# Performance work log

Measured on AMD Instinct MI355X. Metric: run time of the kernel, lower is better.

Reference implementation:

```python
import jax, jax.numpy as jnp
import numpy as np

B, H, S, D = 4, 16, 2048, 64

def setup_inputs() -> dict:
    key = jax.random.key(0)
    kq, kk, kv = jax.random.split(key, 3)
    query = jax.random.normal(kq, (B, H, S, D), dtype=jnp.float32)
    key_t = jax.random.normal(kk, (B, H, S, D), dtype=jnp.float32)
    value = jax.random.normal(kv, (B, H, S, D), dtype=jnp.float32)
    return {"query": query, "key": key_t, "value": value}

def reference(query, key, value):
    d = query.shape[-1]
    scale = 1.0 / jnp.sqrt(jnp.asarray(d, dtype=query.dtype))
    # scores: [B, H, S_q, S_k]
    scores = jnp.einsum('bhqd,bhkd->bhqk', query, key) * scale
    p_attn = jax.nn.softmax(scores, axis=-1)
    # out: [B, H, S_q, D]
    return jnp.einsum('bhqk,bhkd->bhqd', p_attn, value)
```

## Files before the change

### kernel.cpp

```cpp
#include <hip/hip_runtime.h>
#include <hip/hip_bf16.h>


constexpr int Sdim = 2048;
constexpr int Ddim = 64;
constexpr int QBLK = 64;
constexpr int KVBLK = 64;
constexpr int NW = 4;
constexpr int NBH = 64;
constexpr int NT = Sdim / KVBLK;
constexpr float QSCALE = 0.125f * 1.44269504f;
constexpr float DEFER_THR = 11.0f;

typedef __attribute__((ext_vector_type(8))) short short8;
typedef __attribute__((ext_vector_type(4))) float f32x4;
typedef __attribute__((ext_vector_type(4))) unsigned short ushort4v;
typedef __attribute__((ext_vector_type(2))) unsigned int uint2v;

typedef __attribute__((address_space(1))) const unsigned int GU32;
typedef __attribute__((address_space(3))) unsigned int LU32;

__device__ __forceinline__ unsigned short f2bf(float f) {
    union { float f; unsigned int u; } v; v.f = f;
    unsigned int r = v.u + 0x7FFFu + ((v.u >> 16) & 1u);
    return (unsigned short)(r >> 16);
}

__device__ __forceinline__ unsigned int cvt_pk_bf16(float lo, float hi) {
    unsigned int r;
    asm("v_cvt_pk_bf16_f32 %0, %1, %2" : "=v"(r) : "v"(lo), "v"(hi));
    return r;
}

__device__ __forceinline__ void gload_lds16(const unsigned short* g, unsigned short* l) {
    __builtin_amdgcn_global_load_lds((GU32*)g, (LU32*)l, 16, 0, 0);
}

__global__ __launch_bounds__(256)
void prep_k(const float* __restrict__ Kg, unsigned short* __restrict__ Kbf) {
    size_t idx = ((size_t)blockIdx.x * 256 + threadIdx.x) * 4;
    int c0 = (int)(idx & 63);
    size_t row = idx >> 6;
    int swz = ((int)row & 7) << 3;
    float4 f = *(const float4*)(Kg + idx);
    ushort4v h;
    h.x = f2bf(f.x); h.y = f2bf(f.y); h.z = f2bf(f.z); h.w = f2bf(f.w);
    *(ushort4v*)(Kbf + (row << 6) + (c0 ^ swz)) = h;
}

__global__ __launch_bounds__(256)
void prep_v(const float* __restrict__ Vg, unsigned short* __restrict__ Vtb) {
    int bh = blockIdx.x >> 5, t = blockIdx.x & 31;
    const float* src = Vg + ((size_t)bh * Sdim + t * KVBLK) * Ddim;
    unsigned short* dst = Vtb + ((size_t)bh * NT + t) * (Ddim * KVBLK);
    int kv0 = (threadIdx.x & 15) * 4;
    int d0  = (threadIdx.x >> 4) * 4;
    float v[4][4];
#pragma unroll
    for (int j = 0; j < 4; ++j)
        *(float4*)v[j] = *(const float4*)(src + (size_t)(kv0 + j) * Ddim + d0);
#pragma unroll
    for (int i = 0; i < 4; ++i) {
        int d = d0 + i;
        ushort4v h;
        h.x = f2bf(v[0][i]); h.y = f2bf(v[1][i]);
        h.z = f2bf(v[2][i]); h.w = f2bf(v[3][i]);
        *(ushort4v*)(dst + d * KVBLK + (kv0 ^ ((d & 7) << 3))) = h;
    }
}

__global__ __launch_bounds__(256, 4)
void attn_fwd_fast(const float* __restrict__ Qg, const unsigned short* __restrict__ Kbf,
                   const unsigned short* __restrict__ Vtb, float* __restrict__ Og)
{
    __shared__ unsigned short Kt[KVBLK][Ddim];
    __shared__ unsigned short Vt[Ddim][KVBLK];
    __shared__ unsigned short Pt[NW][16][KVBLK];

    const int tid = threadIdx.x;
    const int w   = tid >> 6;
    const int l   = tid & 63;
    const int g   = l >> 4;
    const int q   = l & 15;
    const int swz = (q & 7) << 3;

    const int bh = blockIdx.y;
    const size_t base = (size_t)bh * Sdim * Ddim;
    const int q0 = blockIdx.x * QBLK;

    short8 qf[2];
    {
        const float* qrow = Qg + base + (size_t)(q0 + w * 16 + q) * Ddim;
#pragma unroll
        for (int kc = 0; kc < 2; ++kc) {
            float fv[8];
            *(float4*)(fv)     = *(const float4*)(qrow + kc * 32 + g * 8);
            *(float4*)(fv + 4) = *(const float4*)(qrow + kc * 32 + g * 8 + 4);
            short8 r;
#pragma unroll
            for (int j = 0; j < 8; ++j) r[j] = (short)f2bf(fv[j] * QSCALE);
            qf[kc] = r;
        }
    }

    f32x4 o[4];
#pragma unroll
    for (int dt = 0; dt < 4; ++dt)
#pragma unroll
        for (int r = 0; r < 4; ++r) o[dt][r] = 0.0f;
    float m_run = -INFINITY, l_run = 0.0f;

    for (int t = 0; t < NT; ++t) {
        __syncthreads();
        {
            const unsigned short* ksrc = Kbf + base + (size_t)t * (KVBLK * Ddim);
            const unsigned short* vsrc = Vtb + base + (size_t)t * (KVBLK * Ddim);
            const int eo = w * 512 + l * 8;
            gload_lds16(ksrc + eo,        &Kt[0][0] + w * 512);
            gload_lds16(ksrc + eo + 2048, &Kt[0][0] + w * 512 + 2048);
            gload_lds16(vsrc + eo,        &Vt[0][0] + w * 512);
            gload_lds16(vsrc + eo + 2048, &Vt[0][0] + w * 512 + 2048);
        }
        __syncthreads();

        f32x4 sa[4];
#pragma unroll
        for (int nt = 0; nt < 4; ++nt)
#pragma unroll
            for (int r = 0; r < 4; ++r) sa[nt][r] = 0.0f;
        __builtin_amdgcn_s_setprio(1);
#pragma unroll
        for (int kc = 0; kc < 2; ++kc)
#pragma unroll
            for (int nt = 0; nt < 4; ++nt) {
                const short8 kf = *(const short8*)&Kt[nt * 16 + q][(kc * 32 + g * 8) ^ swz];
                sa[nt] = __builtin_amdgcn_mfma_f32_16x16x32_bf16(kf, qf[kc], sa[nt], 0, 0, 0);
            }
        __builtin_amdgcn_s_setprio(0);

        float mx = sa[0][0];
#pragma unroll
        for (int nt = 0; nt < 4; ++nt)
#pragma unroll
            for (int r = 0; r < 4; ++r) mx = fmaxf(mx, sa[nt][r]);
        mx = fmaxf(mx, __shfl_xor(mx, 16));
        mx = fmaxf(mx, __shfl_xor(mx, 32));

        float p[4][4];
        float s = 0.0f;
        if (__all(mx - m_run <= DEFER_THR)) {
#pragma unroll
            for (int nt = 0; nt < 4; ++nt)
#pragma unroll
                for (int r = 0; r < 4; ++r) {
                    float e = exp2f(sa[nt][r] - m_run);
                    p[nt][r] = e; s += e;
                }
            s += __shfl_xor(s, 16);
            s += __shfl_xor(s, 32);
            l_run += s;
        } else {
            float mnew = fmaxf(m_run, mx);
            float fr = exp2f(m_run - mnew);
            m_run = mnew;
#pragma unroll
            for (int nt = 0; nt < 4; ++nt)
#pragma unroll
                for (int r = 0; r < 4; ++r) {
                    float e = exp2f(sa[nt][r] - mnew);
                    p[nt][r] = e; s += e;
                }
            s += __shfl_xor(s, 16);
            s += __shfl_xor(s, 32);
            l_run = l_run * fr + s;
            float frb[4];
#pragma unroll
            for (int r = 0; r < 4; ++r) frb[r] = __shfl(fr, 4 * g + r);
#pragma unroll
            for (int dt = 0; dt < 4; ++dt)
#pragma unroll
                for (int r = 0; r < 4; ++r) o[dt][r] *= frb[r];
        }

#pragma unroll
        for (int nt = 0; nt < 4; ++nt) {
            uint2v pp;
            pp.x = cvt_pk_bf16(p[nt][0], p[nt][1]);
            pp.y = cvt_pk_bf16(p[nt][2], p[nt][3]);
            *(uint2v*)&Pt[w][q][(nt * 16 + 4 * g) ^ swz] = pp;
        }

        __builtin_amdgcn_s_setprio(1);
#pragma unroll
        for (int kc = 0; kc < 2; ++kc) {
            const short8 pa = *(const short8*)&Pt[w][q][(kc * 32 + g * 8) ^ swz];
#pragma unroll
            for (int dt = 0; dt < 4; ++dt) {
                const short8 vf = *(const short8*)&Vt[dt * 16 + q][(kc * 32 + g * 8) ^ swz];
                o[dt] = __builtin_amdgcn_mfma_f32_16x16x32_bf16(pa, vf, o[dt], 0, 0, 0);
            }
        }
        __builtin_amdgcn_s_setprio(0);
    }

    float inv = 1.0f / l_run;
    float invb[4];
#pragma unroll
    for (int r = 0; r < 4; ++r) invb[r] = __shfl(inv, 4 * g + r);
#pragma unroll
    for (int r = 0; r < 4; ++r) {
        float* orow = Og + base + (size_t)(q0 + w * 16 + 4 * g + r) * Ddim;
#pragma unroll
        for (int dt = 0; dt < 4; ++dt) orow[dt * 16 + q] = o[dt][r] * invb[r];
    }
}

__global__ __launch_bounds__(256, 4)
void attn_fwd_slow(const float* __restrict__ Qg, const float* __restrict__ Kg,
                   const float* __restrict__ Vg, float* __restrict__ Og)
{
    __shared__ unsigned short Kt[KVBLK][Ddim];
    __shared__ unsigned short Vt[Ddim][KVBLK];
    __shared__ unsigned short Pt[NW][16][KVBLK];

    const int tid = threadIdx.x;
    const int w   = tid >> 6;
    const int l   = tid & 63;
    const int g   = l >> 4;
    const int q   = l & 15;
    const int swz = (q & 7) << 3;

    const size_t base = (size_t)blockIdx.y * Sdim * Ddim;
    const int q0 = blockIdx.x * QBLK;

    short8 qf[2];
    {
        const float* qrow = Qg + base + (size_t)(q0 + w * 16 + q) * Ddim;
#pragma unroll
        for (int kc = 0; kc < 2; ++kc) {
            float fv[8];
            *(float4*)(fv)     = *(const float4*)(qrow + kc * 32 + g * 8);
            *(float4*)(fv + 4) = *(const float4*)(qrow + kc * 32 + g * 8 + 4);
            short8 r;
#pragma unroll
            for (int j = 0; j < 8; ++j) r[j] = (short)f2bf(fv[j] * QSCALE);
            qf[kc] = r;
        }
    }

    f32x4 o[4];
#pragma unroll
    for (int dt = 0; dt < 4; ++dt)
#pragma unroll
        for (int r = 0; r < 4; ++r) o[dt][r] = 0.0f;
    float m_run = -INFINITY, l_run = 0.0f;

    for (int t = 0; t < NT; ++t) {
        __syncthreads();
        {
            const float* Ksrc = Kg + base + (size_t)t * KVBLK * Ddim;
            const float* Vsrc = Vg + base + (size_t)t * KVBLK * Ddim;
#pragma unroll
            for (int it = 0; it < 4; ++it) {
                int idx = it * 1024 + tid * 4;
                int r = idx >> 6, c = idx & 63;
                float4 kf4 = *(const float4*)(Ksrc + idx);
                ushort4v hk;
                hk.x = f2bf(kf4.x); hk.y = f2bf(kf4.y);
                hk.z = f2bf(kf4.z); hk.w = f2bf(kf4.w);
                *(ushort4v*)&Kt[r][c ^ ((r & 7) << 3)] = hk;
            }
            {
                const int d = l;
                const int vswz = (d & 7) << 3;
#pragma unroll
                for (int i = 0; i < 4; ++i) {
                    int kv0 = w * 16 + i * 4;
                    float a0 = Vsrc[(size_t)(kv0 + 0) * Ddim + d];
                    float a1 = Vsrc[(size_t)(kv0 + 1) * Ddim + d];
                    float a2 = Vsrc[(size_t)(kv0 + 2) * Ddim + d];
                    float a3 = Vsrc[(size_t)(kv0 + 3) * Ddim + d];
                    ushort4v hv;
                    hv.x = f2bf(a0); hv.y = f2bf(a1);
                    hv.z = f2bf(a2); hv.w = f2bf(a3);
                    *(ushort4v*)&Vt[d][kv0 ^ vswz] = hv;
                }
            }
        }
        __syncthreads();

        f32x4 sa[4];
#pragma unroll
        for (int nt = 0; nt < 4; ++nt)
#pragma unroll
            for (int r = 0; r < 4; ++r) sa[nt][r] = 0.0f;
#pragma unroll
        for (int kc = 0; kc < 2; ++kc)
#pragma unroll
            for (int nt = 0; nt < 4; ++nt) {
                const short8 kf = *(const short8*)&Kt[nt * 16 + q][(kc * 32 + g * 8) ^ swz];
                sa[nt] = __builtin_amdgcn_mfma_f32_16x16x32_bf16(kf, qf[kc], sa[nt], 0, 0, 0);
            }

        float mx = sa[0][0];
#pragma unroll
        for (int nt = 0; nt < 4; ++nt)
#pragma unroll
            for (int r = 0; r < 4; ++r) mx = fmaxf(mx, sa[nt][r]);
        mx = fmaxf(mx, __shfl_xor(mx, 16));
        mx = fmaxf(mx, __shfl_xor(mx, 32));
        float mnew = fmaxf(m_run, mx);
        float fr = exp2f(m_run - mnew);
        m_run = mnew;

        float p[4][4];
        float s = 0.0f;
#pragma unroll
        for (int nt = 0; nt < 4; ++nt)
#pragma unroll
            for (int r = 0; r < 4; ++r) {
                float e = exp2f(sa[nt][r] - mnew);
                p[nt][r] = e; s += e;
            }
        s += __shfl_xor(s, 16);
        s += __shfl_xor(s, 32);
        l_run = l_run * fr + s;

#pragma unroll
        for (int nt = 0; nt < 4; ++nt) {
            uint2v pp;
            pp.x = cvt_pk_bf16(p[nt][0], p[nt][1]);
            pp.y = cvt_pk_bf16(p[nt][2], p[nt][3]);
            *(uint2v*)&Pt[w][q][(nt * 16 + 4 * g) ^ swz] = pp;
        }

        float frb[4];
#pragma unroll
        for (int r = 0; r < 4; ++r) frb[r] = __shfl(fr, 4 * g + r);
#pragma unroll
        for (int dt = 0; dt < 4; ++dt)
#pragma unroll
            for (int r = 0; r < 4; ++r) o[dt][r] *= frb[r];

#pragma unroll
        for (int kc = 0; kc < 2; ++kc) {
            const short8 pa = *(const short8*)&Pt[w][q][(kc * 32 + g * 8) ^ swz];
#pragma unroll
            for (int dt = 0; dt < 4; ++dt) {
                const short8 vf = *(const short8*)&Vt[dt * 16 + q][(kc * 32 + g * 8) ^ swz];
                o[dt] = __builtin_amdgcn_mfma_f32_16x16x32_bf16(pa, vf, o[dt], 0, 0, 0);
            }
        }
    }

    float inv = 1.0f / l_run;
    float invb[4];
#pragma unroll
    for (int r = 0; r < 4; ++r) invb[r] = __shfl(inv, 4 * g + r);
#pragma unroll
    for (int r = 0; r < 4; ++r) {
        float* orow = Og + base + (size_t)(q0 + w * 16 + 4 * g + r) * Ddim;
#pragma unroll
        for (int dt = 0; dt < 4; ++dt) orow[dt * 16 + q] = o[dt][r] * invb[r];
    }
}

extern "C" void kernel_launch(void* const* d_in, const int* in_sizes, int n_in,
                              void* d_out, int out_size, void* d_ws, size_t ws_size,
                              hipStream_t stream) {
    const float* Q = (const float*)d_in[0];
    const float* K = (const float*)d_in[1];
    const float* V = (const float*)d_in[2];
    float* O = (float*)d_out;
    const size_t elems = (size_t)NBH * Sdim * Ddim;
    const size_t need  = elems * 2 * 2;
    dim3 grid(Sdim / QBLK, NBH);
    if (ws_size >= need) {
        unsigned short* Kbf = (unsigned short*)d_ws;
        unsigned short* Vtb = Kbf + elems;
        prep_k<<<dim3((unsigned)(elems / 4 / 256)), dim3(256), 0, stream>>>(K, Kbf);
        prep_v<<<dim3(NBH * NT), dim3(256), 0, stream>>>(V, Vtb);
        attn_fwd_fast<<<grid, dim3(256), 0, stream>>>(Q, Kbf, Vtb, O);
    } else {
        attn_fwd_slow<<<grid, dim3(256), 0, stream>>>(Q, K, V, O);
    }
}
```

Before: 257.3 us.

## Keep P in registers by permuting V layout, fold max into MFMA init

Re-lays out the transposed V in prep_v, now staged through LDS, so that the S-tile accumulator fragment can be packed directly as the A operand of the PV MFMA. This removes the per-tile P round trip through shared memory and its LDS buffer. The running max is subtracted by seeding the QK accumulator with -m_run, and the row-sum reduction is deferred to the end. Occupancy hint is raised to 8 blocks per CU, which risks register pressure.

```diff
diff --git a/kernel.cpp b/kernel.cpp
--- a/kernel.cpp
+++ b/kernel.cpp
@@ -15,7 +15,6 @@
 typedef __attribute__((ext_vector_type(8))) short short8;
 typedef __attribute__((ext_vector_type(4))) float f32x4;
 typedef __attribute__((ext_vector_type(4))) unsigned short ushort4v;
-typedef __attribute__((ext_vector_type(2))) unsigned int uint2v;
 
 typedef __attribute__((address_space(1))) const unsigned int GU32;
 typedef __attribute__((address_space(3))) unsigned int LU32;
@@ -50,32 +49,46 @@
 
 __global__ __launch_bounds__(256)
 void prep_v(const float* __restrict__ Vg, unsigned short* __restrict__ Vtb) {
+    __shared__ unsigned short Vl[KVBLK][Ddim + 4];
     int bh = blockIdx.x >> 5, t = blockIdx.x & 31;
     const float* src = Vg + ((size_t)bh * Sdim + t * KVBLK) * Ddim;
     unsigned short* dst = Vtb + ((size_t)bh * NT + t) * (Ddim * KVBLK);
-    int kv0 = (threadIdx.x & 15) * 4;
-    int d0  = (threadIdx.x >> 4) * 4;
-    float v[4][4];
-#pragma unroll
-    for (int j = 0; j < 4; ++j)
-        *(float4*)v[j] = *(const float4*)(src + (size_t)(kv0 + j) * Ddim + d0);
-#pragma unroll
-    for (int i = 0; i < 4; ++i) {
-        int d = d0 + i;
-        ushort4v h;
-        h.x = f2bf(v[0][i]); h.y = f2bf(v[1][i]);
-        h.z = f2bf(v[2][i]); h.w = f2bf(v[3][i]);
-        *(ushort4v*)(dst + d * KVBLK + (kv0 ^ ((d & 7) << 3))) = h;
-    }
-}
-
-__global__ __launch_bounds__(256, 4)
+
+    {
+        int kv = threadIdx.x >> 2;
+        int dq = (threadIdx.x & 3) * 16;
+#pragma unroll
+        for (int i = 0; i < 4; ++i) {
+            float4 f = *(const float4*)(src + (size_t)kv * Ddim + dq + 4 * i);
+            ushort4v h;
+            h.x = f2bf(f.x); h.y = f2bf(f.y); h.z = f2bf(f.z); h.w = f2bf(f.w);
+            *(ushort4v*)&Vl[kv][dq + 4 * i] = h;
+        }
+    }
+    __syncthreads();
+    {
+        int d  = threadIdx.x >> 2;
+        int sc = (threadIdx.x & 3) * 16;
+        int swzd = (d & 7) << 3;
+#pragma unroll
+        for (int u = 0; u < 4; ++u) {
+            int s0 = sc + 4 * u;
+            int kc = s0 >> 5, g = (s0 >> 3) & 3, h = (s0 >> 2) & 1;
+            int kvb = 32 * kc + 16 * h + 4 * g;
+            ushort4v o;
+            o.x = Vl[kvb + 0][d]; o.y = Vl[kvb + 1][d];
+            o.z = Vl[kvb + 2][d]; o.w = Vl[kvb + 3][d];
+            *(ushort4v*)(dst + (size_t)d * KVBLK + (s0 ^ swzd)) = o;
+        }
+    }
+}
+
+__global__ __launch_bounds__(256, 8)
 void attn_fwd_fast(const float* __restrict__ Qg, const unsigned short* __restrict__ Kbf,
                    const unsigned short* __restrict__ Vtb, float* __restrict__ Og)
 {
     __shared__ unsigned short Kt[KVBLK][Ddim];
     __shared__ unsigned short Vt[Ddim][KVBLK];
-    __shared__ unsigned short Pt[NW][16][KVBLK];
 
     const int tid = threadIdx.x;
     const int w   = tid >> 6;
@@ -108,7 +121,10 @@
     for (int dt = 0; dt < 4; ++dt)
 #pragma unroll
         for (int r = 0; r < 4; ++r) o[dt][r] = 0.0f;
-    float m_run = -INFINITY, l_run = 0.0f;
+    float m_run = 0.0f;
+    float l_part = 0.0f;
+
+    union PU { unsigned int u[4]; short8 s8; };
 
     for (int t = 0; t < NT; ++t) {
         __syncthreads();
@@ -127,7 +143,7 @@
 #pragma unroll
         for (int nt = 0; nt < 4; ++nt)
 #pragma unroll
-            for (int r = 0; r < 4; ++r) sa[nt][r] = 0.0f;
+            for (int r = 0; r < 4; ++r) sa[nt][r] = -m_run;
         __builtin_amdgcn_s_setprio(1);
 #pragma unroll
         for (int kc = 0; kc < 2; ++kc)
@@ -138,41 +154,39 @@
             }
         __builtin_amdgcn_s_setprio(0);
 
-        float mx = sa[0][0];
-#pragma unroll
-        for (int nt = 0; nt < 4; ++nt)
-#pragma unroll
-            for (int r = 0; r < 4; ++r) mx = fmaxf(mx, sa[nt][r]);
+        f32x4 m4 = sa[0];
+#pragma unroll
+        for (int nt = 1; nt < 4; ++nt)
+#pragma unroll
+            for (int r = 0; r < 4; ++r) m4[r] = fmaxf(m4[r], sa[nt][r]);
+        float mx = fmaxf(fmaxf(m4[0], m4[1]), fmaxf(m4[2], m4[3]));
         mx = fmaxf(mx, __shfl_xor(mx, 16));
         mx = fmaxf(mx, __shfl_xor(mx, 32));
 
-        float p[4][4];
-        float s = 0.0f;
-        if (__all(mx - m_run <= DEFER_THR)) {
-#pragma unroll
-            for (int nt = 0; nt < 4; ++nt)
-#pragma unroll
-                for (int r = 0; r < 4; ++r) {
-                    float e = exp2f(sa[nt][r] - m_run);
-                    p[nt][r] = e; s += e;
-                }
-            s += __shfl_xor(s, 16);
-            s += __shfl_xor(s, 32);
-            l_run += s;
+        PU pa[2];
+        float ts = 0.0f;
+        if (__all(mx <= DEFER_THR)) {
+#pragma unroll
+            for (int nt = 0; nt < 4; ++nt) {
+                float e0 = exp2f(sa[nt][0]), e1 = exp2f(sa[nt][1]);
+                float e2 = exp2f(sa[nt][2]), e3 = exp2f(sa[nt][3]);
+                ts += (e0 + e1) + (e2 + e3);
+                pa[nt >> 1].u[(nt & 1) * 2 + 0] = cvt_pk_bf16(e0, e1);
+                pa[nt >> 1].u[(nt & 1) * 2 + 1] = cvt_pk_bf16(e2, e3);
+            }
+            l_part += ts;
         } else {
-            float mnew = fmaxf(m_run, mx);
-            float fr = exp2f(m_run - mnew);
-            m_run = mnew;
-#pragma unroll
-            for (int nt = 0; nt < 4; ++nt)
-#pragma unroll
-                for (int r = 0; r < 4; ++r) {
-                    float e = exp2f(sa[nt][r] - mnew);
-                    p[nt][r] = e; s += e;
-                }
-            s += __shfl_xor(s, 16);
-            s += __shfl_xor(s, 32);
-            l_run = l_run * fr + s;
+            float fr = exp2f(-mx);
+            m_run += mx;
+#pragma unroll
+            for (int nt = 0; nt < 4; ++nt) {
+                float e0 = exp2f(sa[nt][0] - mx), e1 = exp2f(sa[nt][1] - mx);
+                float e2 = exp2f(sa[nt][2] - mx), e3 = exp2f(sa[nt][3] - mx);
+                ts += (e0 + e1) + (e2 + e3);
+                pa[nt >> 1].u[(nt & 1) * 2 + 0] = cvt_pk_bf16(e0, e1);
+                pa[nt >> 1].u[(nt & 1) * 2 + 1] = cvt_pk_bf16(e2, e3);
+            }
+            l_part = l_part * fr + ts;
             float frb[4];
 #pragma unroll
             for (int r = 0; r < 4; ++r) frb[r] = __shfl(fr, 4 * g + r);
@@ -182,28 +196,20 @@
                 for (int r = 0; r < 4; ++r) o[dt][r] *= frb[r];
         }
 
-#pragma unroll
-        for (int nt = 0; nt < 4; ++nt) {
-            uint2v pp;
-            pp.x = cvt_pk_bf16(p[nt][0], p[nt][1]);
-            pp.y = cvt_pk_bf16(p[nt][2], p[nt][3]);
-            *(uint2v*)&Pt[w][q][(nt * 16 + 4 * g) ^ swz] = pp;
-        }
-
         __builtin_amdgcn_s_setprio(1);
 #pragma unroll
-        for (int kc = 0; kc < 2; ++kc) {
-            const short8 pa = *(const short8*)&Pt[w][q][(kc * 32 + g * 8) ^ swz];
+        for (int kc = 0; kc < 2; ++kc)
 #pragma unroll
             for (int dt = 0; dt < 4; ++dt) {
                 const short8 vf = *(const short8*)&Vt[dt * 16 + q][(kc * 32 + g * 8) ^ swz];
-                o[dt] = __builtin_amdgcn_mfma_f32_16x16x32_bf16(pa, vf, o[dt], 0, 0, 0);
-            }
-        }
+                o[dt] = __builtin_amdgcn_mfma_f32_16x16x32_bf16(pa[kc].s8, vf, o[dt], 0, 0, 0);
+            }
         __builtin_amdgcn_s_setprio(0);
     }
 
-    float inv = 1.0f / l_run;
+    l_part += __shfl_xor(l_part, 16);
+    l_part += __shfl_xor(l_part, 32);
+    float inv = 1.0f / l_part;
     float invb[4];
 #pragma unroll
     for (int r = 0; r < 4; ++r) invb[r] = __shfl(inv, 4 * g + r);
@@ -214,6 +220,8 @@
         for (int dt = 0; dt < 4; ++dt) orow[dt * 16 + q] = o[dt][r] * invb[r];
     }
 }
+
+typedef __attribute__((ext_vector_type(2))) unsigned int uint2v;
 
 __global__ __launch_bounds__(256, 4)
 void attn_fwd_slow(const float* __restrict__ Qg, const float* __restrict__ Kg,
@@ -344,11 +352,11 @@
 
 #pragma unroll
         for (int kc = 0; kc < 2; ++kc) {
-            const short8 pa = *(const short8*)&Pt[w][q][(kc * 32 + g * 8) ^ swz];
+            const short8 pf = *(const short8*)&Pt[w][q][(kc * 32 + g * 8) ^ swz];
 #pragma unroll
             for (int dt = 0; dt < 4; ++dt) {
                 const short8 vf = *(const short8*)&Vt[dt * 16 + q][(kc * 32 + g * 8) ^ swz];
-                o[dt] = __builtin_amdgcn_mfma_f32_16x16x32_bf16(pa, vf, o[dt], 0, 0, 0);
+                o[dt] = __builtin_amdgcn_mfma_f32_16x16x32_bf16(pf, vf, o[dt], 0, 0, 0);
             }
         }
     }
```

After: 508.1 us. 97.5% more time.
